# Kernel tuning notes

Hardware: AMD Instinct MI355X
Metric: run time of the kernel (lower is better)

The kernel has to match this reference:

```python
import jax, jax.numpy as jnp
import numpy as np
from jax import lax

B, F, N, C = 1024, 256, 65536, 1000
SOURCE_CLASSES = 751
TEMP = 0.05
MOMENTUM = 0.2


def setup_inputs() -> dict:
    key = jax.random.key(0)
    k1, k2, k3, k4 = jax.random.split(key, 4)
    inputs = jax.random.normal(k1, (B, F), dtype=jnp.float32)
    # indexes in [1, N] so that (indexes - 1) are all valid -> the boolean mask
    # `inds = indexes >= 0` keeps every row (static shapes under jit)
    indexes = jax.random.randint(k2, (B,), 1, N + 1, dtype=jnp.int32)
    features = jax.random.normal(k3, (N, F), dtype=jnp.float32)
    features = features / jnp.linalg.norm(features, axis=1, keepdims=True)  # bank stores unit rows
    labels = jax.random.randint(k4, (N,), 0, C, dtype=jnp.int32)
    return {"inputs": inputs, "indexes": indexes, "features": features, "labels": labels}


def _forward(inputs, idx, features, labels):
    # F.normalize(inputs, dim=1)
    x = inputs / jnp.linalg.norm(inputs, axis=1, keepdims=True)           # [B, F]
    logits = (x @ features.T) / TEMP                                      # [B, N]
    targets = labels[idx]                                                 # [B]
    # sim.index_add_(0, labels, inputs.t()) -> per-class column sums
    sim = jax.ops.segment_sum(logits.T, labels, num_segments=C)           # [C, B]
    nums = jax.ops.segment_sum(jnp.ones((N,), jnp.float32), labels, num_segments=C)  # [C]
    mask = nums > 0
    sim = sim / jnp.where(mask, nums, 1.0)[:, None]                       # per-class mean
    # masked softmax over classes (faithful to original: plain exp, +eps denominator)
    exps = jnp.exp(sim.T) * mask[None, :].astype(jnp.float32)            # [B, C]
    p = exps / (exps.sum(axis=1, keepdims=True) + 1e-6)
    logp = jnp.log(p + 1e-6)
    # F.nll_loss(..., ignore_index=source_classes-1)
    valid = (targets != SOURCE_CLASSES - 1).astype(jnp.float32)
    nll = -jnp.take_along_axis(logp, targets[:, None], axis=1)[:, 0]
    loss = jnp.sum(nll * valid) / jnp.maximum(valid.sum(), 1.0)
    return loss, x


def reference(inputs, indexes, features, labels):
    idx = indexes - 1
    idx = jnp.where(idx == 5554, SOURCE_CLASSES - 1, idx)  # is_source=True special case
    loss, x = _forward(inputs, idx, features, labels)
    # HM.backward's per-sample sequential momentum scatter update + renorm of the bank.
    # Order-dependent on duplicate indices -> inherently sequential -> lax.scan.
    def step(feats, xy):
        xi, yi = xy
        row = MOMENTUM * feats[yi] + (1.0 - MOMENTUM) * xi
        row = row / jnp.linalg.norm(row)
        return feats.at[yi].set(row), None

    new_features, _ = lax.scan(step, features, (x, idx))
    return loss, new_features
```

## Files before the change

### kernel.cpp

```cpp
#include <hip/hip_runtime.h>
#include <math.h>

#define Bn   1024
#define Fdim 256
#define Nn   65536
#define Cn   1000
#define INV_TEMP 20.0f
#define MOM  0.2f

struct WS {
  float x[Bn * Fdim];
  float meanP[Fdim * Cn];
  float mask[Cn];
  float sumExp[Bn];
  float tExp[Bn];
  int   idx[Bn];
  int   targets[Bn];
  int   counts[Cn];
  int   offsets[Cn];
  int   cursor[Cn];
  int   list[Nn];
};

__global__ __launch_bounds__(64) void k1_norm(const float* __restrict__ inputs,
                                              const int* __restrict__ indexes,
                                              const int* __restrict__ labels,
                                              float* __restrict__ x,
                                              int* __restrict__ idx, int* __restrict__ targets,
                                              int* __restrict__ counts,
                                              float* __restrict__ sumExp) {
  int b = blockIdx.x, t = threadIdx.x;
  int g = b * 64 + t;
  if (g < Cn) counts[g] = 0;
  if (g < Bn) sumExp[g] = 0.f;
  float4 v = *(const float4*)&inputs[b * Fdim + t * 4];
  float s = v.x * v.x + v.y * v.y + v.z * v.z + v.w * v.w;
#pragma unroll
  for (int o = 32; o > 0; o >>= 1) s += __shfl_xor(s, o, 64);
  float inv = 1.0f / sqrtf(s);
  v.x *= inv; v.y *= inv; v.z *= inv; v.w *= inv;
  *(float4*)&x[b * Fdim + t * 4] = v;
  if (t == 0) {
    int i0 = indexes[b] - 1;
    if (i0 == 5554) i0 = 750;
    idx[b] = i0;
    targets[b] = labels[i0];
  }
}

__global__ __launch_bounds__(256) void k2_count(const int* __restrict__ labels,
                                                int* __restrict__ counts) {
  int t = blockIdx.x * blockDim.x + threadIdx.x;
  int4 l = *(const int4*)&labels[t * 4];
  atomicAdd(&counts[l.x], 1);
  atomicAdd(&counts[l.y], 1);
  atomicAdd(&counts[l.z], 1);
  atomicAdd(&counts[l.w], 1);
}

__global__ void k3_scan(const int* __restrict__ counts, int* __restrict__ offsets,
                        int* __restrict__ cursor) {
  __shared__ int s[1024];
  int t = threadIdx.x;
  int v = (t < Cn) ? counts[t] : 0;
  s[t] = v;
  __syncthreads();
  for (int o = 1; o < 1024; o <<= 1) {
    int a = (t >= o) ? s[t - o] : 0;
    __syncthreads();
    s[t] += a;
    __syncthreads();
  }
  if (t < Cn) {
    int off = s[t] - v;
    offsets[t] = off;
    cursor[t] = off;
  }
}

__global__ __launch_bounds__(256) void k4_fill(const int* __restrict__ labels,
                                               int* __restrict__ cursor,
                                               int* __restrict__ list) {
  int t = blockIdx.x * blockDim.x + threadIdx.x;
  int4 l = *(const int4*)&labels[t * 4];
  int n = t * 4;
  list[atomicAdd(&cursor[l.x], 1)] = n;
  list[atomicAdd(&cursor[l.y], 1)] = n + 1;
  list[atomicAdd(&cursor[l.z], 1)] = n + 2;
  list[atomicAdd(&cursor[l.w], 1)] = n + 3;
}

__global__ __launch_bounds__(256) void k5_classsum(const float* __restrict__ features,
                                                   const int* __restrict__ list,
                                                   const int* __restrict__ offsets,
                                                   const int* __restrict__ counts,
                                                   float* __restrict__ meanP,
                                                   float* __restrict__ mask,
                                                   float* __restrict__ out1) {
  int c = blockIdx.x, t = threadIdx.x, w = t >> 6, lane = t & 63;
  int off = offsets[c], cnt = counts[c];
  __shared__ int mlds[512];
  __shared__ float partial[4][256];
  float4 acc = {0.f, 0.f, 0.f, 0.f};
  for (int base = 0; base < cnt; base += 512) {
    int m = min(512, cnt - base);
    for (int i = t; i < m; i += 256) mlds[i] = list[off + base + i];
    __syncthreads();
    int i = w;
    for (; i + 4 < m; i += 8) {
      int n0 = mlds[i], n1 = mlds[i + 4];
      float4 v0 = *(const float4*)&features[n0 * Fdim + lane * 4];
      float4 v1 = *(const float4*)&features[n1 * Fdim + lane * 4];
      acc.x += v0.x + v1.x; acc.y += v0.y + v1.y;
      acc.z += v0.z + v1.z; acc.w += v0.w + v1.w;
      float* o0 = &out1[n0 * Fdim + lane * 4];
      o0[0] = v0.x; o0[1] = v0.y; o0[2] = v0.z; o0[3] = v0.w;
      float* o1 = &out1[n1 * Fdim + lane * 4];
      o1[0] = v1.x; o1[1] = v1.y; o1[2] = v1.z; o1[3] = v1.w;
    }
    for (; i < m; i += 4) {
      int n = mlds[i];
      float4 v = *(const float4*)&features[n * Fdim + lane * 4];
      acc.x += v.x; acc.y += v.y; acc.z += v.z; acc.w += v.w;
      float* o = &out1[n * Fdim + lane * 4];
      o[0] = v.x; o[1] = v.y; o[2] = v.z; o[3] = v.w;
    }
    __syncthreads();
  }
  *(float4*)&partial[w][lane * 4] = acc;
  __syncthreads();
  float s = partial[0][t] + partial[1][t] + partial[2][t] + partial[3][t];
  meanP[((t >> 2) * Cn + c) * 4 + (t & 3)] = (cnt > 0) ? s / (float)cnt : 0.f;
  if (t == 0) mask[c] = (cnt > 0) ? 1.f : 0.f;
}

#define BBT 4
__global__ __launch_bounds__(256) void k6_matmul(const float* __restrict__ x,
                                                 const float* __restrict__ meanP,
                                                 const float* __restrict__ mask,
                                                 const int* __restrict__ targets,
                                                 float* __restrict__ sumExp,
                                                 float* __restrict__ tExp) {
  int b0 = blockIdx.x * BBT;
  int c  = blockIdx.y * 256 + threadIdx.x;
  int lane = threadIdx.x & 63;
  bool cv = (c < Cn);
  int cc = cv ? c : 0;
  float acc[BBT];
#pragma unroll
  for (int bb = 0; bb < BBT; bb++) acc[bb] = 0.f;
  const float* xb = x + b0 * Fdim;
#pragma unroll 4
  for (int f4 = 0; f4 < Fdim / 4; f4++) {
    float4 mv = *(const float4*)&meanP[(f4 * Cn + cc) * 4];
#pragma unroll
    for (int bb = 0; bb < BBT; bb++) {
      float4 xv = *(const float4*)&xb[bb * Fdim + f4 * 4];
      acc[bb] = fmaf(xv.x, mv.x, acc[bb]);
      acc[bb] = fmaf(xv.y, mv.y, acc[bb]);
      acc[bb] = fmaf(xv.z, mv.z, acc[bb]);
      acc[bb] = fmaf(xv.w, mv.w, acc[bb]);
    }
  }
  float msk = cv ? mask[cc] : 0.f;
#pragma unroll
  for (int bb = 0; bb < BBT; bb++) {
    float e = msk * __expf(acc[bb] * INV_TEMP);
    float s = e;
#pragma unroll
    for (int o = 32; o > 0; o >>= 1) s += __shfl_down(s, o, 64);
    if (lane == 0) atomicAdd(&sumExp[b0 + bb], s);
    int tgt = targets[b0 + bb];
    if (cv && tgt == c) tExp[b0 + bb] = e;
  }
}

__global__ __launch_bounds__(256) void k8_update(const float* __restrict__ features,
                                                 const float* __restrict__ x,
                                                 const int* __restrict__ idx,
                                                 const float* __restrict__ sumExp,
                                                 const float* __restrict__ tExp,
                                                 const int* __restrict__ targets,
                                                 float* __restrict__ out,
                                                 float* __restrict__ out1) {
  int t = threadIdx.x;
  if (blockIdx.x == 256) {
    float a = 0.f, bsum = 0.f;
#pragma unroll
    for (int k = 0; k < 4; k++) {
      int b = t + k * 256;
      float S = sumExp[b], tE = tExp[b];
      float nll = -logf(tE / (S + 1e-6f) + 1e-6f);
      float valid = (targets[b] != 750) ? 1.f : 0.f;
      a += nll * valid; bsum += valid;
    }
#pragma unroll
    for (int o = 32; o > 0; o >>= 1) {
      a += __shfl_down(a, o, 64);
      bsum += __shfl_down(bsum, o, 64);
    }
    __shared__ float ra[4], rb[4];
    if ((t & 63) == 0) { ra[t >> 6] = a; rb[t >> 6] = bsum; }
    __syncthreads();
    if (t == 0) {
      float sa = ra[0] + ra[1] + ra[2] + ra[3];
      float sb = rb[0] + rb[1] + rb[2] + rb[3];
      out[0] = sa / fmaxf(sb, 1.f);
    }
    return;
  }
  __shared__ int ilds[Bn];
  for (int i = t; i < Bn; i += 256) ilds[i] = idx[i];
  __syncthreads();
  int wid = t >> 6, lane = t & 63;
  int b = blockIdx.x * 4 + wid;
  int y = ilds[b];
  for (int base = 0; base < b; base += 64) {
    int j = base + lane;
    bool hit = (j < b) && (ilds[j] == y);
    if (__any(hit)) return;
  }
  float4 r = *(const float4*)&features[y * Fdim + lane * 4];
  for (int base = (b >> 6) << 6; base < Bn; base += 64) {
    int k = base + lane;
    bool hit = (k >= b) && (ilds[k] == y);
    unsigned long long mbits = __ballot(hit);
    while (mbits) {
      int p = __ffsll(mbits) - 1;
      mbits &= mbits - 1;
      int kk = base + p;
      float4 xv = *(const float4*)&x[kk * Fdim + lane * 4];
      r.x = MOM * r.x + (1.f - MOM) * xv.x;
      r.y = MOM * r.y + (1.f - MOM) * xv.y;
      r.z = MOM * r.z + (1.f - MOM) * xv.z;
      r.w = MOM * r.w + (1.f - MOM) * xv.w;
      float ss = r.x * r.x + r.y * r.y + r.z * r.z + r.w * r.w;
#pragma unroll
      for (int o = 32; o > 0; o >>= 1) ss += __shfl_xor(ss, o, 64);
      float inv = 1.0f / sqrtf(ss);
      r.x *= inv; r.y *= inv; r.z *= inv; r.w *= inv;
    }
  }
  int base2 = y * Fdim + lane * 4;
  out1[base2 + 0] = r.x;
  out1[base2 + 1] = r.y;
  out1[base2 + 2] = r.z;
  out1[base2 + 3] = r.w;
}

extern "C" void kernel_launch(void* const* d_in, const int* in_sizes, int n_in,
                              void* d_out, int out_size, void* d_ws, size_t ws_size,
                              hipStream_t stream) {
  const float* inputs   = (const float*)d_in[0];
  const int*   indexes  = (const int*)d_in[1];
  const float* features = (const float*)d_in[2];
  const int*   labels   = (const int*)d_in[3];
  float* out = (float*)d_out;
  WS* w = (WS*)d_ws;

  k1_norm<<<Bn, 64, 0, stream>>>(inputs, indexes, labels, w->x, w->idx, w->targets,
                                 w->counts, w->sumExp);
  k2_count<<<Nn / 1024, 256, 0, stream>>>(labels, w->counts);
  k3_scan<<<1, 1024, 0, stream>>>(w->counts, w->offsets, w->cursor);
  k4_fill<<<Nn / 1024, 256, 0, stream>>>(labels, w->cursor, w->list);
  k5_classsum<<<Cn, 256, 0, stream>>>(features, w->list, w->offsets, w->counts,
                                      w->meanP, w->mask, out + 1);
  k6_matmul<<<dim3(Bn / BBT, 4), 256, 0, stream>>>(w->x, w->meanP, w->mask, w->targets,
                                                   w->sumExp, w->tExp);
  k8_update<<<Bn / 4 + 1, 256, 0, stream>>>(features, w->x, w->idx, w->sumExp, w->tExp,
                                            w->targets, out, out + 1);
}
```

Before: 198.6 us.

## Replace per-class gather with flat segmented reduction over sorted list plus atomics

The per-class gather kernel (one block per class, uneven counts) is replaced by a flat kernel where each wavefront walks 16 consecutive entries of the class-sorted list, runs segmented sums and flushes partials to a class-major accumulator with float atomics. A small pack kernel then divides by the counts and writes the transposed meanP layout plus the mask. The zero-initialisation of counts and sumExp moves from k1 into a single memset that also clears the new accumulator. This is meant to balance load across the GPU and raise memory-level parallelism, at the cost of an extra launch, atomic traffic and a summation order that is no longer deterministic.

```diff
diff --git a/kernel.cpp b/kernel.cpp
--- a/kernel.cpp
+++ b/kernel.cpp
@@ -12,27 +12,23 @@
   float x[Bn * Fdim];
   float meanP[Fdim * Cn];
   float mask[Cn];
-  float sumExp[Bn];
   float tExp[Bn];
   int   idx[Bn];
   int   targets[Bn];
-  int   counts[Cn];
   int   offsets[Cn];
   int   cursor[Cn];
   int   list[Nn];
+  float meanC[Cn * Fdim];
+  int   counts[Cn];
+  float sumExp[Bn];
 };
 
 __global__ __launch_bounds__(64) void k1_norm(const float* __restrict__ inputs,
                                               const int* __restrict__ indexes,
                                               const int* __restrict__ labels,
                                               float* __restrict__ x,
-                                              int* __restrict__ idx, int* __restrict__ targets,
-                                              int* __restrict__ counts,
-                                              float* __restrict__ sumExp) {
+                                              int* __restrict__ idx, int* __restrict__ targets) {
   int b = blockIdx.x, t = threadIdx.x;
-  int g = b * 64 + t;
-  if (g < Cn) counts[g] = 0;
-  if (g < Bn) sumExp[g] = 0.f;
   float4 v = *(const float4*)&inputs[b * Fdim + t * 4];
   float s = v.x * v.x + v.y * v.y + v.z * v.z + v.w * v.w;
 #pragma unroll
@@ -90,47 +86,57 @@
   list[atomicAdd(&cursor[l.w], 1)] = n + 3;
 }
 
-__global__ __launch_bounds__(256) void k5_classsum(const float* __restrict__ features,
-                                                   const int* __restrict__ list,
-                                                   const int* __restrict__ offsets,
-                                                   const int* __restrict__ counts,
-                                                   float* __restrict__ meanP,
-                                                   float* __restrict__ mask,
-                                                   float* __restrict__ out1) {
-  int c = blockIdx.x, t = threadIdx.x, w = t >> 6, lane = t & 63;
-  int off = offsets[c], cnt = counts[c];
-  __shared__ int mlds[512];
-  __shared__ float partial[4][256];
+__global__ __launch_bounds__(256) void k5_fused(const float* __restrict__ features,
+                                                const int* __restrict__ list,
+                                                const int* __restrict__ labels,
+                                                float* __restrict__ meanC,
+                                                float* __restrict__ out1) {
+  int w = blockIdx.x * 4 + (threadIdx.x >> 6);
+  int lane = threadIdx.x & 63;
+  int e0 = w * 16;
   float4 acc = {0.f, 0.f, 0.f, 0.f};
-  for (int base = 0; base < cnt; base += 512) {
-    int m = min(512, cnt - base);
-    for (int i = t; i < m; i += 256) mlds[i] = list[off + base + i];
-    __syncthreads();
-    int i = w;
-    for (; i + 4 < m; i += 8) {
-      int n0 = mlds[i], n1 = mlds[i + 4];
-      float4 v0 = *(const float4*)&features[n0 * Fdim + lane * 4];
-      float4 v1 = *(const float4*)&features[n1 * Fdim + lane * 4];
-      acc.x += v0.x + v1.x; acc.y += v0.y + v1.y;
-      acc.z += v0.z + v1.z; acc.w += v0.w + v1.w;
-      float* o0 = &out1[n0 * Fdim + lane * 4];
-      o0[0] = v0.x; o0[1] = v0.y; o0[2] = v0.z; o0[3] = v0.w;
-      float* o1 = &out1[n1 * Fdim + lane * 4];
-      o1[0] = v1.x; o1[1] = v1.y; o1[2] = v1.z; o1[3] = v1.w;
-    }
-    for (; i < m; i += 4) {
-      int n = mlds[i];
-      float4 v = *(const float4*)&features[n * Fdim + lane * 4];
-      acc.x += v.x; acc.y += v.y; acc.z += v.z; acc.w += v.w;
-      float* o = &out1[n * Fdim + lane * 4];
-      o[0] = v.x; o[1] = v.y; o[2] = v.z; o[3] = v.w;
-    }
-    __syncthreads();
-  }
-  *(float4*)&partial[w][lane * 4] = acc;
-  __syncthreads();
-  float s = partial[0][t] + partial[1][t] + partial[2][t] + partial[3][t];
-  meanP[((t >> 2) * Cn + c) * 4 + (t & 3)] = (cnt > 0) ? s / (float)cnt : 0.f;
+  int cur = -1;
+#pragma unroll
+  for (int bh = 0; bh < 2; bh++) {
+    int r[8], cc[8];
+#pragma unroll
+    for (int j = 0; j < 8; j++) r[j] = list[e0 + bh * 8 + j];
+#pragma unroll
+    for (int j = 0; j < 8; j++) cc[j] = labels[r[j]];
+    float4 v[8];
+#pragma unroll
+    for (int j = 0; j < 8; j++)
+      v[j] = *(const float4*)&features[r[j] * Fdim + lane * 4];
+#pragma unroll
+    for (int j = 0; j < 8; j++) {
+      float* o = &out1[r[j] * Fdim + lane * 4];
+      o[0] = v[j].x; o[1] = v[j].y; o[2] = v[j].z; o[3] = v[j].w;
+      if (cc[j] != cur) {
+        if (cur >= 0) {
+          float* p = &meanC[cur * Fdim + lane * 4];
+          atomicAdd(p + 0, acc.x); atomicAdd(p + 1, acc.y);
+          atomicAdd(p + 2, acc.z); atomicAdd(p + 3, acc.w);
+        }
+        acc.x = 0.f; acc.y = 0.f; acc.z = 0.f; acc.w = 0.f;
+        cur = cc[j];
+      }
+      acc.x += v[j].x; acc.y += v[j].y; acc.z += v[j].z; acc.w += v[j].w;
+    }
+  }
+  float* p = &meanC[cur * Fdim + lane * 4];
+  atomicAdd(p + 0, acc.x); atomicAdd(p + 1, acc.y);
+  atomicAdd(p + 2, acc.z); atomicAdd(p + 3, acc.w);
+}
+
+__global__ __launch_bounds__(256) void k5t_pack(const float* __restrict__ meanC,
+                                                const int* __restrict__ counts,
+                                                float* __restrict__ meanP,
+                                                float* __restrict__ mask) {
+  int c = blockIdx.x, t = threadIdx.x;
+  int cnt = counts[c];
+  float rc = (cnt > 0) ? 1.0f / (float)cnt : 0.f;
+  float s = meanC[c * Fdim + t];
+  meanP[((t >> 2) * Cn + c) * 4 + (t & 3)] = s * rc;
   if (t == 0) mask[c] = (cnt > 0) ? 1.f : 0.f;
 }
 
@@ -258,13 +264,13 @@
   float* out = (float*)d_out;
   WS* w = (WS*)d_ws;
 
-  k1_norm<<<Bn, 64, 0, stream>>>(inputs, indexes, labels, w->x, w->idx, w->targets,
-                                 w->counts, w->sumExp);
+  hipMemsetAsync(w->meanC, 0, (size_t)(Cn * Fdim + Cn + Bn) * 4, stream);
+  k1_norm<<<Bn, 64, 0, stream>>>(inputs, indexes, labels, w->x, w->idx, w->targets);
   k2_count<<<Nn / 1024, 256, 0, stream>>>(labels, w->counts);
   k3_scan<<<1, 1024, 0, stream>>>(w->counts, w->offsets, w->cursor);
   k4_fill<<<Nn / 1024, 256, 0, stream>>>(labels, w->cursor, w->list);
-  k5_classsum<<<Cn, 256, 0, stream>>>(features, w->list, w->offsets, w->counts,
-                                      w->meanP, w->mask, out + 1);
+  k5_fused<<<Nn / 64, 256, 0, stream>>>(features, w->list, labels, w->meanC, out + 1);
+  k5t_pack<<<Cn, 256, 0, stream>>>(w->meanC, w->counts, w->meanP, w->mask);
   k6_matmul<<<dim3(Bn / BBT, 4), 256, 0, stream>>>(w->x, w->meanP, w->mask, w->targets,
                                                    w->sumExp, w->tExp);
   k8_update<<<Bn / 4 + 1, 256, 0, stream>>>(features, w->x, w->idx, w->sumExp, w->tExp,
```

New measurement: 196.6 us. Within noise of the previous version (-1.0%).
